# Optimization experiments

Hardware: AMD Instinct MI355X
Metric: run time of the kernel (lower is better)

## Reference

```python
import jax, jax.numpy as jnp
import numpy as np

KSIZE = 3
SCALE = 2


def setup_inputs() -> dict:
    key = jax.random.key(0)
    k1, k2, k3, k4 = jax.random.split(key, 4)
    B, C, H, W = 8, 3, 512, 512
    h, w = H // SCALE, W // SCALE
    return {
        "images": jax.random.uniform(k1, (B, C, H, W), jnp.float32),
        "kernels": jax.random.uniform(k2, (B, KSIZE ** 2, h, w), jnp.float32),
        "offsets_x": jax.random.uniform(k3, (B, KSIZE ** 2, h, w), jnp.float32),
        "offsets_y": jax.random.uniform(k4, (B, KSIZE ** 2, h, w), jnp.float32),
    }


def _softround(x, alpha=1.0):
    two_pi = 2.0 * jnp.pi
    return x - alpha * (jnp.sin(two_pi * x) / two_pi)


def _batch_bli(im, x, y):
    # im: [B, H, W, 3] channel-last; x, y: [B, N] float coords
    B, N = x.shape
    x0 = jnp.floor(x).astype(jnp.int32)
    x1 = x0 + 1
    y0 = jnp.floor(y).astype(jnp.int32)
    y1 = y0 + 1
    # original clamps x by im.shape[2] and y by im.shape[1] (square images)
    x0 = jnp.clip(x0, 0, im.shape[2] - 1)
    x1 = jnp.clip(x1, 0, im.shape[2] - 1)
    y0 = jnp.clip(y0, 0, im.shape[1] - 1)
    y1 = jnp.clip(y1, 0, im.shape[1] - 1)
    bidx = jnp.arange(B)[:, None]
    # vectorized gather of the four corners; flatten like torch.cat of [3]-vectors
    Ia = im[bidx, x0, y0].reshape(-1)  # [B*N*3]
    Ib = im[bidx, x0, y1].reshape(-1)
    Ic = im[bidx, x1, y0].reshape(-1)
    Id = im[bidx, x1, y1].reshape(-1)
    scale_w = (1.0 / ((x1 - x0) * (y1 - y0))).reshape(-1)  # [B*N]
    # faithful to the original's (scrambling) reshape semantics
    m1 = jnp.concatenate([x1 - x, x - x0], axis=1).astype(jnp.float32)  # [B, 2N]
    m1 = jnp.tile(m1.reshape(B * N, 1, 1, 2), (1, 2, 1, 1))             # [BN,2,1,2]
    m2 = jnp.stack([Ib, Ia, Id, Ic], axis=1).reshape(B * N, 2, 2, 3)    # [BN,2,2,3]
    m3 = jnp.concatenate([y1 - y, y - y0], axis=1).astype(jnp.float32)
    m3 = m3.reshape(B * N, 1, 2, 1)                                     # [BN,1,2,1]
    t = jnp.matmul(m1, m2).transpose(0, 3, 2, 1)  # [BN,3,1,2]
    out = jnp.matmul(t, m3).reshape(B * N, 3)     # [BN,3]
    return scale_w[:, None] * out


def reference(images, kernels, offsets_x, offsets_y):
    B = images.shape[0]
    h, w = images.shape[2] // SCALE, images.shape[3] // SCALE
    kernels = kernels.transpose(0, 2, 3, 1)      # [B,h,w,9]
    ox = offsets_x.transpose(0, 2, 3, 1)         # [B,h,w,9]
    oy = offsets_y.transpose(0, 2, 3, 1)
    u = jnp.arange(h, dtype=jnp.float32) + 0.5 * SCALE - 0.5
    kx = jnp.repeat(jnp.arange(KSIZE), KSIZE).astype(jnp.float32)  # 0,0,0,1,1,1,2,2,2
    ky = jnp.tile(jnp.arange(KSIZE), KSIZE).astype(jnp.float32)    # 0,1,2,0,1,2,0,1,2
    # original broadcasts u.reshape(h,1) over the w axis (requires h == w)
    coords_x = ox + KSIZE / 2 + kx + u[:, None]
    coords_y = oy + KSIZE / 2 + ky + u[:, None]
    im = images.transpose(0, 2, 3, 1)  # [B,H,W,3]
    pix = _batch_bli(im, coords_x.reshape(B, -1), coords_y.reshape(B, -1))
    pix_hr = pix.reshape(B, h, w, KSIZE ** 2, 3)
    out = jnp.sum(kernels[..., None] * pix_hr, axis=-2)  # [B,h,w,3]
    return _softround(out * 255.0)
```

## Files before the change

### kernel.cpp

```cpp
#include <hip/hip_runtime.h>
#include <math.h>

#define BATCH 8
#define HI 512
#define WI 512
#define HO 256
#define WO 256
#define PLANE (HI*WI)
#define OPIX (HO*WO)
#define LROWS 68
#define LCOLS 10
#define LSTRIDE 33
#define LDS_FLOATS (LROWS*LSTRIDE)

__global__ __launch_bounds__(256, 4) void downsampler_kernel(
    const float* __restrict__ images,
    const float* __restrict__ kernels,
    const float* __restrict__ offx,
    const float* __restrict__ offy,
    float* __restrict__ out)
{
    __shared__ float simg[LDS_FLOATS];

    const int blk  = blockIdx.x;
    const int b    = blk >> 7;
    const int ihx  = (blk >> 2) & 31;
    const int w0   = (blk & 3) << 6;
    const int tid  = threadIdx.x;
    const int lane = tid & 63;
    const int g    = tid >> 6;
    const int iw   = w0 + lane;

    {
        const float* imb = images + (size_t)b * 3 * PLANE;
        const int total = LROWS * LCOLS * 3;
        for (int i = tid; i < total; i += 256) {
            const int ch  = i / (LROWS * LCOLS);
            const int rem = i - ch * (LROWS * LCOLS);
            const int rr  = rem / LCOLS;
            const int cr  = rem - rr * LCOLS;
            const int r = w0 + 2 + rr;
            int c = r - 4 + cr;
            c = c < 0 ? 0 : c;
            simg[rr * LSTRIDE + cr * 3 + ch] = imb[ch * PLANE + r * WI + c];
        }
    }
    __syncthreads();

    const bool flip = (ihx < 16);
    const float* offxb = offx    + (size_t)b * 9 * OPIX;
    const float* offyb = offy    + (size_t)b * 9 * OPIX;
    const float* kernb = kernels + (size_t)b * 9 * OPIX;

    const float uu_own = (float)iw + 0.5f;
    const float uu_s0  = (float)((2 * iw) & 255) + 0.5f;
    const float uu_s1  = uu_s0 + 1.0f;

    const float TWO_PI_INV = 0.15915494309189533577f;

    #pragma unroll
    for (int p = 0; p < 2; ++p) {
        const int ih = (ihx << 3) + (g << 1) + p;
        const int pl = ih * WO + iw;
        const int pix2 = pl & (OPIX / 2 - 1);

        float2 vx[9], vy[9];
        #pragma unroll
        for (int ks = 0; ks < 9; ++ks) {
            vx[ks] = ((const float2*)(offxb + ks * OPIX))[pix2];
            vy[ks] = ((const float2*)(offyb + ks * OPIX))[pix2];
        }
        float wx[18], wy[18];
        #pragma unroll
        for (int t = 0; t < 18; ++t) {
            const int sel = (t >= 9) ? 1 : 0;
            const int ks  = t - 9 * sel;
            const float uu  = sel ? uu_s1 : uu_s0;
            const float oxv = sel ? vx[ks].y : vx[ks].x;
            const float oyv = sel ? vy[ks].y : vy[ks].x;
            const float kxf = (float)(ks / 3);
            const float kyf = (float)(ks - 3 * (ks / 3));
            const float cxx = ((oxv + 1.5f) + kxf) + uu;
            const float cyy = ((oyv + 1.5f) + kyf) + uu;
            const float fx = cxx - floorf(cxx);
            const float fy = cyy - floorf(cyy);
            wx[t] = flip ? (1.0f - fx) : fx;
            wy[t] = flip ? (1.0f - fy) : fy;
        }

        float acc0 = 0.f, acc1 = 0.f, acc2 = 0.f;
        #pragma unroll
        for (int k = 0; k < 9; ++k) {
            const float kxf = (float)(k / 3);
            const float kyf = (float)(k - 3 * (k / 3));
            const float cx = ((offxb[k * OPIX + pl] + 1.5f) + kxf) + uu_own;
            const float cy = ((offyb[k * OPIX + pl] + 1.5f) + kyf) + uu_own;
            const int x0 = (int)floorf(cx);
            const int y0 = (int)floorf(cy);

            const float* r0 = &simg[(x0 - 2 - w0) * LSTRIDE];
            const float* r1 = r0 + LSTRIDE;
            const int c00 = (y0 - x0 + 4) * 3;
            const int c01 = c00 + 3;
            const int c10 = c00 - 3;
            const int c11 = c00;

            const float Ia0 = r0[c00 + 0], Ia1 = r0[c00 + 1], Ia2 = r0[c00 + 2];
            const float Ib0 = r0[c01 + 0], Ib1 = r0[c01 + 1], Ib2 = r0[c01 + 2];
            const float Ic0 = r1[c10 + 0], Ic1 = r1[c10 + 1], Ic2 = r1[c10 + 2];
            const float Id0 = r1[c11 + 0], Id1 = r1[c11 + 1], Id2 = r1[c11 + 2];

            const float w0w = wx[2 * k], w1w = wx[2 * k + 1];
            const float v0w = wy[2 * k], v1w = wy[2 * k + 1];
            const float w0v0 = w0w * v0w, w1v0 = w1w * v0w;
            const float w0v1 = w0w * v1w, w1v1 = w1w * v1w;

            const float p0 = w0v0 * Ib0 + w1v0 * Ic0 + w0v1 * Id1 + w1v1 * Ia2;
            const float p1 = w0v0 * Ia0 + w1v0 * Ib1 + w0v1 * Ic1 + w1v1 * Id2;
            const float p2 = w0v0 * Id0 + w1v0 * Ia1 + w0v1 * Ib2 + w1v1 * Ic2;

            const float kv = kernb[k * OPIX + pl];
            acc0 += kv * p0;
            acc1 += kv * p1;
            acc2 += kv * p2;
        }

        const size_t obase = ((size_t)b * OPIX + (size_t)pl) * 3;
        const float z0 = acc0 * 255.0f;
        const float z1 = acc1 * 255.0f;
        const float z2 = acc2 * 255.0f;
        const float r0s = z0 - rintf(z0);
        const float r1s = z1 - rintf(z1);
        const float r2s = z2 - rintf(z2);
        out[obase + 0] = z0 - __builtin_amdgcn_sinf(r0s) * TWO_PI_INV;
        out[obase + 1] = z1 - __builtin_amdgcn_sinf(r1s) * TWO_PI_INV;
        out[obase + 2] = z2 - __builtin_amdgcn_sinf(r2s) * TWO_PI_INV;
    }
}

extern "C" void kernel_launch(void* const* d_in, const int* in_sizes, int n_in,
                              void* d_out, int out_size, void* d_ws, size_t ws_size,
                              hipStream_t stream) {
    const float* images  = (const float*)d_in[0];
    const float* kernels = (const float*)d_in[1];
    const float* offx    = (const float*)d_in[2];
    const float* offy    = (const float*)d_in[3];
    float* out = (float*)d_out;

    dim3 grid(BATCH * 32 * 4);
    dim3 block(256);
    hipLaunchKernelGGL(downsampler_kernel, grid, block, 0, stream,
                       images, kernels, offx, offy, out);
}
```

Measured before the change: 116.2 us.

## Pack image tile as float4 in LDS and hoist all global loads upfront

Stores the three channels of each staged pixel as one padded float4 in shared memory, so each bilinear corner becomes a single 128-bit LDS read instead of three scalar reads. All offset, kernel and shuffled-offset global loads for both output rows are issued before any compute, so their memory latency overlaps. The fractional-weight computation is folded into the main loop. The extra register pressure is met by lowering the launch-bounds occupancy hint from 4 to 3 blocks, which may reduce latency hiding.

```diff
diff --git a/kernel.cpp b/kernel.cpp
--- a/kernel.cpp
+++ b/kernel.cpp
@@ -10,17 +10,16 @@
 #define OPIX (HO*WO)
 #define LROWS 68
 #define LCOLS 10
-#define LSTRIDE 33
-#define LDS_FLOATS (LROWS*LSTRIDE)
+#define LQ 11
 
-__global__ __launch_bounds__(256, 4) void downsampler_kernel(
+__global__ __launch_bounds__(256, 3) void downsampler_kernel(
     const float* __restrict__ images,
     const float* __restrict__ kernels,
     const float* __restrict__ offx,
     const float* __restrict__ offy,
     float* __restrict__ out)
 {
-    __shared__ float simg[LDS_FLOATS];
+    __shared__ float4 simg[LROWS * LQ];
 
     const int blk  = blockIdx.x;
     const int b    = blk >> 7;
@@ -33,16 +32,16 @@
 
     {
         const float* imb = images + (size_t)b * 3 * PLANE;
-        const int total = LROWS * LCOLS * 3;
+        const int total = LROWS * LCOLS;
         for (int i = tid; i < total; i += 256) {
-            const int ch  = i / (LROWS * LCOLS);
-            const int rem = i - ch * (LROWS * LCOLS);
-            const int rr  = rem / LCOLS;
-            const int cr  = rem - rr * LCOLS;
-            const int r = w0 + 2 + rr;
-            int c = r - 4 + cr;
+            const int row = i / LCOLS;
+            const int col = i - row * LCOLS;
+            const int r = w0 + 2 + row;
+            int c = r - 4 + col;
             c = c < 0 ? 0 : c;
-            simg[rr * LSTRIDE + cr * 3 + ch] = imb[ch * PLANE + r * WI + c];
+            const float* src = imb + r * WI + c;
+            simg[row * LQ + col] =
+                make_float4(src[0], src[PLANE], src[2 * PLANE], 0.0f);
         }
     }
     __syncthreads();
@@ -58,71 +57,85 @@
 
     const float TWO_PI_INV = 0.15915494309189533577f;
 
+    float  ox[2][9], oy[2][9], kv[2][9];
+    float2 sx[2][9], sy[2][9];
+    int    pls[2];
     #pragma unroll
     for (int p = 0; p < 2; ++p) {
         const int ih = (ihx << 3) + (g << 1) + p;
         const int pl = ih * WO + iw;
+        pls[p] = pl;
         const int pix2 = pl & (OPIX / 2 - 1);
-
-        float2 vx[9], vy[9];
         #pragma unroll
         for (int ks = 0; ks < 9; ++ks) {
-            vx[ks] = ((const float2*)(offxb + ks * OPIX))[pix2];
-            vy[ks] = ((const float2*)(offyb + ks * OPIX))[pix2];
+            ox[p][ks] = offxb[ks * OPIX + pl];
+            oy[p][ks] = offyb[ks * OPIX + pl];
+            kv[p][ks] = kernb[ks * OPIX + pl];
+            sx[p][ks] = ((const float2*)(offxb + ks * OPIX))[pix2];
+            sy[p][ks] = ((const float2*)(offyb + ks * OPIX))[pix2];
         }
-        float wx[18], wy[18];
-        #pragma unroll
-        for (int t = 0; t < 18; ++t) {
-            const int sel = (t >= 9) ? 1 : 0;
-            const int ks  = t - 9 * sel;
-            const float uu  = sel ? uu_s1 : uu_s0;
-            const float oxv = sel ? vx[ks].y : vx[ks].x;
-            const float oyv = sel ? vy[ks].y : vy[ks].x;
-            const float kxf = (float)(ks / 3);
-            const float kyf = (float)(ks - 3 * (ks / 3));
-            const float cxx = ((oxv + 1.5f) + kxf) + uu;
-            const float cyy = ((oyv + 1.5f) + kyf) + uu;
-            const float fx = cxx - floorf(cxx);
-            const float fy = cyy - floorf(cyy);
-            wx[t] = flip ? (1.0f - fx) : fx;
-            wy[t] = flip ? (1.0f - fy) : fy;
-        }
+    }
 
+    #pragma unroll
+    for (int p = 0; p < 2; ++p) {
+        const int pl = pls[p];
         float acc0 = 0.f, acc1 = 0.f, acc2 = 0.f;
+
         #pragma unroll
         for (int k = 0; k < 9; ++k) {
             const float kxf = (float)(k / 3);
             const float kyf = (float)(k - 3 * (k / 3));
-            const float cx = ((offxb[k * OPIX + pl] + 1.5f) + kxf) + uu_own;
-            const float cy = ((offyb[k * OPIX + pl] + 1.5f) + kyf) + uu_own;
+            const float cx = ((ox[p][k] + 1.5f) + kxf) + uu_own;
+            const float cy = ((oy[p][k] + 1.5f) + kyf) + uu_own;
             const int x0 = (int)floorf(cx);
             const int y0 = (int)floorf(cy);
 
-            const float* r0 = &simg[(x0 - 2 - w0) * LSTRIDE];
-            const float* r1 = r0 + LSTRIDE;
-            const int c00 = (y0 - x0 + 4) * 3;
-            const int c01 = c00 + 3;
-            const int c10 = c00 - 3;
-            const int c11 = c00;
+            const int rowrel = x0 - 2 - w0;
+            const int colq   = y0 - x0 + 4;
+            const float4* q0 = &simg[rowrel * LQ];
+            const float4* q1 = q0 + LQ;
+            const float4 Ia = q0[colq];
+            const float4 Ib = q0[colq + 1];
+            const float4 Ic = q1[colq - 1];
+            const float4 Id = q1[colq];
 
-            const float Ia0 = r0[c00 + 0], Ia1 = r0[c00 + 1], Ia2 = r0[c00 + 2];
-            const float Ib0 = r0[c01 + 0], Ib1 = r0[c01 + 1], Ib2 = r0[c01 + 2];
-            const float Ic0 = r1[c10 + 0], Ic1 = r1[c10 + 1], Ic2 = r1[c10 + 2];
-            const float Id0 = r1[c11 + 0], Id1 = r1[c11 + 1], Id2 = r1[c11 + 2];
+            const int ta = 2 * k,      tb = 2 * k + 1;
+            const int sel_a = (ta >= 9) ? 1 : 0;
+            const int sel_b = (tb >= 9) ? 1 : 0;
+            const int ks_a = ta - 9 * sel_a;
+            const int ks_b = tb - 9 * sel_b;
+            const float uu_a = sel_a ? uu_s1 : uu_s0;
+            const float uu_b = sel_b ? uu_s1 : uu_s0;
+            const float oxa = sel_a ? sx[p][ks_a].y : sx[p][ks_a].x;
+            const float oya = sel_a ? sy[p][ks_a].y : sy[p][ks_a].x;
+            const float oxb2 = sel_b ? sx[p][ks_b].y : sx[p][ks_b].x;
+            const float oyb2 = sel_b ? sy[p][ks_b].y : sy[p][ks_b].x;
+            const float kxa = (float)(ks_a / 3), kya = (float)(ks_a - 3 * (ks_a / 3));
+            const float kxb = (float)(ks_b / 3), kyb = (float)(ks_b - 3 * (ks_b / 3));
 
-            const float w0w = wx[2 * k], w1w = wx[2 * k + 1];
-            const float v0w = wy[2 * k], v1w = wy[2 * k + 1];
+            const float cxa = ((oxa + 1.5f) + kxa) + uu_a;
+            const float cya = ((oya + 1.5f) + kya) + uu_a;
+            const float cxb = ((oxb2 + 1.5f) + kxb) + uu_b;
+            const float cyb = ((oyb2 + 1.5f) + kyb) + uu_b;
+            const float fxa = cxa - floorf(cxa);
+            const float fya = cya - floorf(cya);
+            const float fxb = cxb - floorf(cxb);
+            const float fyb = cyb - floorf(cyb);
+            const float w0w = flip ? (1.0f - fxa) : fxa;
+            const float w1w = flip ? (1.0f - fxb) : fxb;
+            const float v0w = flip ? (1.0f - fya) : fya;
+            const float v1w = flip ? (1.0f - fyb) : fyb;
+
             const float w0v0 = w0w * v0w, w1v0 = w1w * v0w;
             const float w0v1 = w0w * v1w, w1v1 = w1w * v1w;
 
-            const float p0 = w0v0 * Ib0 + w1v0 * Ic0 + w0v1 * Id1 + w1v1 * Ia2;
-            const float p1 = w0v0 * Ia0 + w1v0 * Ib1 + w0v1 * Ic1 + w1v1 * Id2;
-            const float p2 = w0v0 * Id0 + w1v0 * Ia1 + w0v1 * Ib2 + w1v1 * Ic2;
+            const float p0 = w0v0 * Ib.x + w1v0 * Ic.x + w0v1 * Id.y + w1v1 * Ia.z;
+            const float p1 = w0v0 * Ia.x + w1v0 * Ib.y + w0v1 * Ic.y + w1v1 * Id.z;
+            const float p2 = w0v0 * Id.x + w1v0 * Ia.y + w0v1 * Ib.z + w1v1 * Ic.z;
 
-            const float kv = kernb[k * OPIX + pl];
-            acc0 += kv * p0;
-            acc1 += kv * p1;
-            acc2 += kv * p2;
+            acc0 += kv[p][k] * p0;
+            acc1 += kv[p][k] * p1;
+            acc2 += kv[p][k] * p2;
         }
 
         const size_t obase = ((size_t)b * OPIX + (size_t)pl) * 3;
```

Result: no change. 116.4 us (+0.1%).
